# Performance work log

Hardware: AMD Instinct MI355X
Metric: run time of the kernel (lower is better)

## Reference

```python
import jax, jax.numpy as jnp
import numpy as np


def setup_inputs() -> dict:
    key = jax.random.key(0)
    k1, k2 = jax.random.split(key)
    B, C, H, W = 16, 2, 512, 512
    probs = jax.random.uniform(k1, (B, C, H, W), dtype=jnp.float32)
    gt = jax.random.randint(k2, (B, 1, H, W), 0, 2, dtype=jnp.int32)
    return {"probs": probs, "gt": gt}


def _edt_sq(mask):
    """Exact squared Euclidean distance transform of the background.

    mask: [H, W] bool, True = foreground (gt == 1).
    Returns [H, W] float32: squared distance from each pixel to nearest
    foreground pixel (0 at foreground), matching
    scipy.ndimage.distance_transform_edt(1 - gt)**2.
    Separable algorithm: exact 1D pass along rows (nearest fg row per
    column via cummax/cummin), then min-plus with squared column offsets.
    """
    H, W = mask.shape
    rows = jnp.arange(H, dtype=jnp.float32)[:, None]  # [H, 1]
    BIG = float(2 * (H + W))  # sentinel: farther than any real distance
    # nearest foreground row at-or-above / at-or-below each pixel, per column
    f = jax.lax.cummax(jnp.where(mask, rows, -BIG), axis=0)            # [H, W]
    b = jax.lax.cummin(jnp.where(mask, rows, BIG + H), axis=0, reverse=True)
    d1 = jnp.minimum((rows - f) ** 2, (b - rows) ** 2)  # column-wise sq dist [H, W]
    cols = jnp.arange(W, dtype=jnp.float32)
    jdiff = (cols[:, None] - cols[None, :]) ** 2        # [W_out, W_in]
    # exact 2D: d2[i, j] = min_{j'} (d1[i, j'] + (j - j')^2)
    return jnp.min(d1[:, None, :] + jdiff[None, :, :], axis=-1)  # [H, W]


def reference(probs, gt):
    mask = gt[:, 0].astype(bool)                 # [B, H, W]
    # sequential over batch (lax.map) to bound the [H, W, W] intermediate
    dist = jnp.sqrt(jax.lax.map(_edt_sq, mask))  # [B, H, W]
    return jnp.mean(probs[:, 0] * dist)
```

## Files before the change

kernel.cpp:

```cpp
#include <hip/hip_runtime.h>
#include <math.h>

constexpr int BATCH = 16;
constexpr int H = 512;
constexpr int W = 512;
constexpr int R = 8;
constexpr int ROWS = 16;
constexpr int GRID = BATCH * H / ROWS;
constexpr float INV_N = 1.0f / (float)(16 * 512 * 512);

__global__ __launch_bounds__(512) void boundary_loss_main(
    const float* __restrict__ probs,
    const int* __restrict__ gt,
    float* __restrict__ partial)
{
    const int blk = blockIdx.x;
    const int b = blk >> 5;
    const int i0 = (blk & 31) * ROWS;
    const int j = threadIdx.x;

    const int* colp = gt + (size_t)b * (H * W) + j;

    const float* prow = probs + (size_t)b * 2 * H * W + (size_t)i0 * W + j;
    float p[ROWS];
    #pragma unroll
    for (int r = 0; r < ROWS; ++r) p[r] = prow[r * W];

    unsigned mask = 0;
    #pragma unroll
    for (int k = 0; k < ROWS + 2 * R; ++k) {
        int rr = i0 - R + k;
        rr = max(0, min(H - 1, rr));
        mask |= ((unsigned)colp[rr * W] & 1u) << k;
    }

    int d1v[ROWS];
    #pragma unroll
    for (int r = 0; r < ROWS; ++r) {
        const int ir = i0 + r;
        const int c = R + r;
        const int up_max = ir;
        const int dn_max = H - 1 - ir;
        const unsigned m_up = (c == 31) ? mask : (mask & ((2u << c) - 1));
        const unsigned m_dn = mask >> c;
        int tu = m_up ? (c - (31 - __clz((int)m_up))) : -1;
        int td = m_dn ? (__ffs((int)m_dn) - 1) : -1;
        if (tu < 0 && up_max > c) {
            int t = c + 1;
            while (tu < 0 && t <= up_max) {
                int v[4];
                #pragma unroll
                for (int k = 0; k < 4; ++k)
                    v[k] = colp[(ir - min(t + k, up_max)) * W];
                #pragma unroll
                for (int k = 0; k < 4; ++k)
                    if (tu < 0 && t + k <= up_max && v[k]) tu = t + k;
                t += 4;
            }
        }
        const int dn_reach = 31 - c;
        if (td < 0 && dn_max > dn_reach) {
            int t = dn_reach + 1;
            while (td < 0 && t <= dn_max) {
                int v[4];
                #pragma unroll
                for (int k = 0; k < 4; ++k)
                    v[k] = colp[(ir + min(t + k, dn_max)) * W];
                #pragma unroll
                for (int k = 0; k < 4; ++k)
                    if (td < 0 && t + k <= dn_max && v[k]) td = t + k;
                t += 4;
            }
        }
        const int du = (tu >= 0) ? tu * tu : (ir + 2048) * (ir + 2048);
        const int dd = (td >= 0) ? td * td : (2560 - ir) * (2560 - ir);
        d1v[r] = min(du, dd);
    }

    __shared__ int d1s[ROWS][W];
    #pragma unroll
    for (int r = 0; r < ROWS; ++r) d1s[r][j] = d1v[r];
    __syncthreads();

    float v = 0.0f;
    #pragma unroll
    for (int r = 0; r < ROWS; ++r) {
        int best = d1v[r];
        const int* drow = d1s[r];
        #pragma unroll
        for (int t = 1; t <= 4; ++t) {
            const int tt = t * t;
            const int cl = drow[max(j - t, 0)] + tt;
            const int cr = drow[min(j + t, W - 1)] + tt;
            if (j - t >= 0) best = min(best, cl);
            if (j + t < W)  best = min(best, cr);
        }
        if (best > 25) {
            int t = 5;
            while (t < W && t * t < best) {
                #pragma unroll
                for (int k = 0; k < 2; ++k) {
                    const int tk = t + k;
                    const int tt = tk * tk;
                    const int cl = drow[max(j - tk, 0)] + tt;
                    const int cr = drow[min(j + tk, W - 1)] + tt;
                    if (j - tk >= 0) best = min(best, cl);
                    if (j + tk < W)  best = min(best, cr);
                }
                t += 2;
            }
        }
        v += p[r] * sqrtf((float)best);
    }

    for (int off = 32; off > 0; off >>= 1)
        v += __shfl_down(v, off, 64);
    __shared__ float wsum[8];
    const int lane = j & 63;
    const int wid = j >> 6;
    if (lane == 0) wsum[wid] = v;
    __syncthreads();
    if (j == 0) {
        float s = 0.0f;
        #pragma unroll
        for (int wi = 0; wi < 8; ++wi) s += wsum[wi];
        partial[blk] = s;
    }
}

__global__ __launch_bounds__(512) void boundary_loss_reduce(
    const float* __restrict__ partial,
    float* __restrict__ out)
{
    const int j = threadIdx.x;
    float s = (j < GRID) ? partial[j] : 0.0f;
    for (int off = 32; off > 0; off >>= 1)
        s += __shfl_down(s, off, 64);
    __shared__ float wsum[8];
    const int lane = j & 63;
    const int wid = j >> 6;
    if (lane == 0) wsum[wid] = s;
    __syncthreads();
    if (j == 0) {
        float tot = 0.0f;
        #pragma unroll
        for (int wi = 0; wi < 8; ++wi) tot += wsum[wi];
        out[0] = tot * INV_N;
    }
}

extern "C" void kernel_launch(void* const* d_in, const int* in_sizes, int n_in,
                              void* d_out, int out_size, void* d_ws, size_t ws_size,
                              hipStream_t stream) {
    const float* probs = (const float*)d_in[0];
    const int* gt = (const int*)d_in[1];
    float* out = (float*)d_out;
    float* partial = (float*)d_ws;

    boundary_loss_main<<<dim3(GRID), dim3(W), 0, stream>>>(probs, gt, partial);
    boundary_loss_reduce<<<dim3(1), dim3(512), 0, stream>>>(partial, out);
}
```

Before: 93.13 us.

## Remap column pass to 4 contiguous columns per thread with padded shared windows

The column min-plus pass now assigns each thread four adjacent columns of one row. A thread reads a 12-wide window of the padded shared row with int4 loads and the matching probs with float4 loads, and the padding sentinels remove the boundary checks from the inner loop. The probs loads move after the row pass, gt loads are batched into registers before the mask is built, and block indices are swizzled so neighbouring blocks come from different batch images. This cuts shared and global load instruction counts and branch overhead. In exchange, lanes that need the slow-path far search diverge more, since each thread now handles four pixels serially.

```diff
diff --git a/kernel.cpp b/kernel.cpp
--- a/kernel.cpp
+++ b/kernel.cpp
@@ -7,6 +7,8 @@
 constexpr int R = 8;
 constexpr int ROWS = 16;
 constexpr int GRID = BATCH * H / ROWS;
+constexpr int PADW = W + 8;
+constexpr int BIG = 8000000;
 constexpr float INV_N = 1.0f / (float)(16 * 512 * 512);
 
 __global__ __launch_bounds__(512) void boundary_loss_main(
@@ -14,34 +16,40 @@
     const int* __restrict__ gt,
     float* __restrict__ partial)
 {
-    const int blk = blockIdx.x;
+    const int hw = blockIdx.x;
+    const int blk = ((hw & 63) << 3) | (hw >> 6);
     const int b = blk >> 5;
     const int i0 = (blk & 31) * ROWS;
     const int j = threadIdx.x;
 
     const int* colp = gt + (size_t)b * (H * W) + j;
 
-    const float* prow = probs + (size_t)b * 2 * H * W + (size_t)i0 * W + j;
-    float p[ROWS];
-    #pragma unroll
-    for (int r = 0; r < ROWS; ++r) p[r] = prow[r * W];
-
-    unsigned mask = 0;
+    int wv[ROWS + 2 * R];
     #pragma unroll
     for (int k = 0; k < ROWS + 2 * R; ++k) {
         int rr = i0 - R + k;
         rr = max(0, min(H - 1, rr));
-        mask |= ((unsigned)colp[rr * W] & 1u) << k;
+        wv[k] = colp[rr * W];
+    }
+    unsigned mask = 0;
+    #pragma unroll
+    for (int k = 0; k < ROWS + 2 * R; ++k)
+        mask |= ((unsigned)wv[k] & 1u) << k;
+
+    __shared__ __align__(16) int d1s[ROWS][PADW];
+    if (j < 128) {
+        const int rr = j >> 3, slot = j & 7;
+        const int idx = (slot < 4) ? slot : (W + slot);
+        d1s[rr][idx] = BIG;
     }
 
-    int d1v[ROWS];
     #pragma unroll
     for (int r = 0; r < ROWS; ++r) {
         const int ir = i0 + r;
         const int c = R + r;
         const int up_max = ir;
         const int dn_max = H - 1 - ir;
-        const unsigned m_up = (c == 31) ? mask : (mask & ((2u << c) - 1));
+        const unsigned m_up = mask & ((2u << c) - 1);
         const unsigned m_dn = mask >> c;
         int tu = m_up ? (c - (31 - __clz((int)m_up))) : -1;
         int td = m_dn ? (__ffs((int)m_dn) - 1) : -1;
@@ -74,43 +82,44 @@
         }
         const int du = (tu >= 0) ? tu * tu : (ir + 2048) * (ir + 2048);
         const int dd = (td >= 0) ? td * td : (2560 - ir) * (2560 - ir);
-        d1v[r] = min(du, dd);
+        d1s[r][4 + j] = min(du, dd);
     }
-
-    __shared__ int d1s[ROWS][W];
-    #pragma unroll
-    for (int r = 0; r < ROWS; ++r) d1s[r][j] = d1v[r];
     __syncthreads();
 
+    const float* pbase = probs + (size_t)b * 2 * H * W + (size_t)i0 * W;
     float v = 0.0f;
     #pragma unroll
-    for (int r = 0; r < ROWS; ++r) {
-        int best = d1v[r];
-        const int* drow = d1s[r];
+    for (int pass = 0; pass < 4; ++pass) {
+        const int tau = pass * 512 + j;
+        const int row = tau >> 7;
+        const int jc = (tau & 127) << 2;
+        const int* drow = d1s[row];
+        const int4* qp = (const int4*)(drow + jc);
+        const int4 qa = qp[0], qb = qp[1], qc = qp[2];
+        const int win[12] = {qa.x, qa.y, qa.z, qa.w,
+                             qb.x, qb.y, qb.z, qb.w,
+                             qc.x, qc.y, qc.z, qc.w};
+        const float4 p4 = *(const float4*)(pbase + (size_t)row * W + jc);
+        const float pv[4] = {p4.x, p4.y, p4.z, p4.w};
         #pragma unroll
-        for (int t = 1; t <= 4; ++t) {
-            const int tt = t * t;
-            const int cl = drow[max(j - t, 0)] + tt;
-            const int cr = drow[min(j + t, W - 1)] + tt;
-            if (j - t >= 0) best = min(best, cl);
-            if (j + t < W)  best = min(best, cr);
+        for (int m = 0; m < 4; ++m) {
+            int best = win[4 + m];
+            #pragma unroll
+            for (int t = 1; t <= 4; ++t) {
+                best = min(best, win[4 + m - t] + t * t);
+                best = min(best, win[4 + m + t] + t * t);
+            }
+            if (best > 25) {
+                const int c0 = jc + m;
+                int t = 5;
+                while (t < W && t * t < best) {
+                    if (c0 - t >= 0) best = min(best, drow[4 + c0 - t] + t * t);
+                    if (c0 + t <  W) best = min(best, drow[4 + c0 + t] + t * t);
+                    ++t;
+                }
+            }
+            v += pv[m] * sqrtf((float)best);
         }
-        if (best > 25) {
-            int t = 5;
-            while (t < W && t * t < best) {
-                #pragma unroll
-                for (int k = 0; k < 2; ++k) {
-                    const int tk = t + k;
-                    const int tt = tk * tk;
-                    const int cl = drow[max(j - tk, 0)] + tt;
-                    const int cr = drow[min(j + tk, W - 1)] + tt;
-                    if (j - tk >= 0) best = min(best, cl);
-                    if (j + tk < W)  best = min(best, cr);
-                }
-                t += 2;
-            }
-        }
-        v += p[r] * sqrtf((float)best);
     }
 
     for (int off = 32; off > 0; off >>= 1)
@@ -157,6 +166,6 @@
     float* out = (float*)d_out;
     float* partial = (float*)d_ws;
 
-    boundary_loss_main<<<dim3(GRID), dim3(W), 0, stream>>>(probs, gt, partial);
+    boundary_loss_main<<<dim3(GRID), dim3(512), 0, stream>>>(probs, gt, partial);
     boundary_loss_reduce<<<dim3(1), dim3(512), 0, stream>>>(partial, out);
 }
```

Result: faster. 88.52 us (median of 2 runs) (-5.0%).
